# Kernel optimization log

Hardware: AMD Instinct MI355X
Metric: run time of the kernel (lower is better)

The kernel has to match this reference:

```python
import jax, jax.numpy as jnp
import numpy as np

B, OBS, H, D, E, T, A = 8192, 128, 512, 512, 16, 50, 32
LOG_STD_MIN, LOG_STD_MAX = -20.0, 2.0
ACT_LIMIT = 1.0


def setup_inputs() -> dict:
    key = jax.random.key(0)
    ks = jax.random.split(key, 24)
    s = 0.05  # weight init scale for MLP weights
    f32 = jnp.float32
    return {
        "obs": jax.random.normal(ks[0], (B, OBS), f32),
        "task": jax.random.randint(ks[1], (B,), 0, T),
        "eps": jax.random.normal(ks[2], (B, A), f32),
        # backbone: obs_dim -> 512 -> 512, relu after every layer
        "bW1": jax.random.normal(ks[3], (OBS, H), f32) * s, "bb1": jnp.zeros((H,), f32),
        "bW2": jax.random.normal(ks[4], (H, H), f32) * s, "bb2": jnp.zeros((H,), f32),
        # stacked expert MLPs: 512 -> 512(relu) -> 512(identity), batched over E
        "eW1": jax.random.normal(ks[5], (E, H, D), f32) * s, "eb1": jnp.zeros((E, D), f32),
        "eW2": jax.random.normal(ks[6], (E, D, D), f32) * s, "eb2": jnp.zeros((E, D), f32),
        # attention params (torch.randn init in original)
        "key_mats": jax.random.normal(ks[7], (E, D, D), f32),
        "value_mats": jax.random.normal(ks[8], (E, D, D), f32),
        "task_queries": jax.random.normal(ks[9], (T, D), f32),
        # mu tower: D -> 512(relu) -> act_dim
        "mW1": jax.random.normal(ks[10], (D, H), f32) * s, "mb1": jnp.zeros((H,), f32),
        "mW2": jax.random.normal(ks[11], (H, A), f32) * s, "mb2": jnp.zeros((A,), f32),
        # log_std tower: D -> 512(relu) -> act_dim
        "lW1": jax.random.normal(ks[12], (D, H), f32) * s, "lb1": jnp.zeros((H,), f32),
        "lW2": jax.random.normal(ks[13], (H, A), f32) * s, "lb2": jnp.zeros((A,), f32),
    }


def reference(obs, task, eps, bW1, bb1, bW2, bb2, eW1, eb1, eW2, eb2,
              key_mats, value_mats, task_queries,
              mW1, mb1, mW2, mb2, lW1, lb1, lW2, lb2):
    relu = jax.nn.relu
    # backbone (relu after both layers, incl. output_activation=activation)
    h = relu(obs @ bW1 + bb1)          # [B, H]
    h = relu(h @ bW2 + bb2)            # [B, H]
    # all experts as one batched GEMM (replaces jit.fork per-expert dispatch)
    eo = relu(jnp.einsum('bi,eij->bej', h, eW1) + eb1)   # [B, E, D]
    eo = jnp.einsum('bej,ejk->bek', eo, eW2) + eb2       # [B, E, D]
    # attention-weighted mixture of experts
    vals = jnp.einsum('bei,eij->bej', eo, value_mats)    # [B, E, D]
    keys = jnp.einsum('bei,eij->bej', eo, key_mats)      # [B, E, D]
    q = task_queries[task]                               # [B, D]
    w = jax.nn.softmax(jnp.einsum('bei,bi->be', keys, q), axis=-1)  # [B, E]
    tower = jnp.einsum('be,bei->bi', w, vals)            # [B, D]
    # squashed Gaussian head
    mu = relu(tower @ mW1 + mb1) @ mW2 + mb2             # [B, A]
    log_std = jnp.clip(relu(tower @ lW1 + lb1) @ lW2 + lb2, LOG_STD_MIN, LOG_STD_MAX)
    a = mu + jnp.exp(log_std) * eps                      # rsample with explicit noise
    # Normal log_prob of a = mu + std*eps, summed over action dim
    logp = jnp.sum(-0.5 * eps * eps - log_std - 0.5 * jnp.log(2.0 * jnp.pi), axis=-1)
    # tanh-squash correction
    logp = logp - jnp.sum(2.0 * (jnp.log(2.0) - a - jax.nn.softplus(-2.0 * a)), axis=-1)
    pi = ACT_LIMIT * jnp.tanh(a)
    return (pi, logp)
```

## Files before the change

kernel.cpp:

```cpp
#include <hip/hip_runtime.h>
#include <hip/hip_bf16.h>
#include <cstdint>


typedef _Float16 f16;
typedef _Float16 f16x4 __attribute__((ext_vector_type(4)));
typedef _Float16 f16x8 __attribute__((ext_vector_type(8)));
typedef float f32x4 __attribute__((ext_vector_type(4)));

__device__ __forceinline__ void fsplit(float x, f16& h, f16& l) {
    h = (f16)x;
    l = (f16)(x - (float)h);
}

__device__ __forceinline__ void gload16(const void* g, void* s) {
    __builtin_amdgcn_global_load_lds(
        (const __attribute__((address_space(1))) void*)g,
        (__attribute__((address_space(3))) void*)s, 16, 0, 0);
}

__global__ void split_pairs(const float* __restrict__ x, f16* __restrict__ h,
                            f16* __restrict__ l, int n4) {
    int i = blockIdx.x * 256 + threadIdx.x;
    if (i >= n4) return;
    float4 v = ((const float4*)x)[i];
    float a[4] = {v.x, v.y, v.z, v.w};
    f16x4 hh, ll;
#pragma unroll
    for (int j = 0; j < 4; ++j) { f16 hj, lj; fsplit(a[j], hj, lj); hh[j] = hj; ll[j] = lj; }
    *(f16x4*)&h[(long)i * 4] = hh;
    *(f16x4*)&l[(long)i * 4] = ll;
}

__global__ void transpose_split(const float* __restrict__ W, f16* __restrict__ Th,
                                f16* __restrict__ Tl, int K, int N, long ist, long ost) {
    __shared__ float t[32][33];
    const float* Wb = W + (long)blockIdx.z * ist;
    const int k0 = blockIdx.x * 32, n0 = blockIdx.y * 32;
    const int tid = threadIdx.x;
    const int r = tid >> 3, c4 = (tid & 7) * 4;
    float4 v = *(const float4*)&Wb[(long)(k0 + r) * N + n0 + c4];
    t[r][c4] = v.x; t[r][c4 + 1] = v.y; t[r][c4 + 2] = v.z; t[r][c4 + 3] = v.w;
    __syncthreads();
    f16x4 hh, ll;
#pragma unroll
    for (int j = 0; j < 4; ++j) { f16 hj, lj; fsplit(t[c4 + j][r], hj, lj); hh[j] = hj; ll[j] = lj; }
    long ob = (long)blockIdx.z * ost + (long)(n0 + r) * K + k0 + c4;
    *(f16x4*)&Th[ob] = hh;
    *(f16x4*)&Tl[ob] = ll;
}

__global__ void build_w2t(const float* __restrict__ mW2, const float* __restrict__ lW2,
                          float* __restrict__ W2T) {
    const int i = blockIdx.x * 256 + threadIdx.x;
    const int half = i >> 14, col = (i >> 9) & 31, k = i & 511;
    const float* src = half ? lW2 : mW2;
    W2T[i] = src[k * 32 + col];
}

__global__ void build_bcat(const float* __restrict__ mb1, const float* __restrict__ lb1,
                           float* __restrict__ bcat) {
    const int i = blockIdx.x * 256 + threadIdx.x;
    bcat[i] = (i < 512) ? mb1[i] : lb1[i - 512];
}

template <int OUTM, bool RELU, int AMODE, bool BSINGLE>
__global__ __launch_bounds__(256, AMODE == 0 ? 3 : 4) void gemm_pair(
    const f16* __restrict__ Ah, const f16* __restrict__ Al, int lda, long zsA,
    const f16* __restrict__ Bh, const f16* __restrict__ Bl, int ldb, long zsB,
    const float* __restrict__ bias, long zsBias,
    f16* __restrict__ Ch, f16* __restrict__ Cl, float* __restrict__ Cf,
    int ldc, long zsC, int K,
    const float* __restrict__ wscale,
    const int* __restrict__ task, const float* __restrict__ KQ2,
    float* __restrict__ scores) {
    __shared__ f16 As[AMODE == 0 ? 2 : 1][64][64];
    __shared__ f16 Bs[BSINGLE ? 1 : 2][128][64];
    const int z = blockIdx.z;
    Ah += (long)z * zsA;
    if constexpr (AMODE == 0) Al += (long)z * zsA;
    Bh += (long)z * zsB;
    if constexpr (!BSINGLE) Bl += (long)z * zsB;
    if (bias) bias += (long)z * zsBias;
    if (OUTM <= 1) { Ch += (long)z * zsC; Cl += (long)z * zsC; }
    if (OUTM == 7) { Ch += (long)z * zsC; }
    if (OUTM == 2 || OUTM == 3 || OUTM == 6) { Cf += (long)z * zsC; }
    const int tid = threadIdx.x;
    const int l = tid & 63;
    const int w = tid >> 6;
    const int row0 = blockIdx.x * 64;
    const int col0 = blockIdx.y * 128;
    const int wr = (w >> 1) * 32;
    const int wc = (w & 1) * 64;
    const int grow = l >> 3;
    const int gch = (l & 7) ^ grow;

    f32x4 acc[2][4];
#pragma unroll
    for (int mi = 0; mi < 2; ++mi)
#pragma unroll
        for (int ni = 0; ni < 4; ++ni)
#pragma unroll
            for (int j = 0; j < 4; ++j) acc[mi][ni][j] = 0.f;

    uint4 areg0, areg1; float ascl0, ascl1;
    auto ldA = [&](int k0) {
        const int r0 = w * 16 + grow, r1 = r0 + 8;
        const int scl = l & 7;
        areg0 = *(const uint4*)&Ah[(long)(row0 + r0) * lda + k0 + scl * 8];
        areg1 = *(const uint4*)&Ah[(long)(row0 + r1) * lda + k0 + scl * 8];
        const int e = k0 >> 9;
        ascl0 = wscale[(long)(row0 + r0) * 16 + e];
        ascl1 = wscale[(long)(row0 + r1) * 16 + e];
    };
    auto wrA = [&]() {
        const int scl = l & 7;
#pragma unroll
        for (int h = 0; h < 2; ++h) {
            const int r = w * 16 + grow + h * 8;
            const float s = h ? ascl1 : ascl0;
            f16x8 v = h ? *(f16x8*)&areg1 : *(f16x8*)&areg0;
#pragma unroll
            for (int j = 0; j < 8; ++j) v[j] = (f16)((float)v[j] * s);
            *(uint4*)&As[0][r][(scl ^ (r & 7)) * 8] = *(uint4*)&v;
        }
    };

    if constexpr (AMODE == 2) ldA(0);
    for (int k0 = 0; k0 < K; k0 += 64) {
        __syncthreads();
        if constexpr (AMODE == 2) {
            wrA();
            if (k0 + 64 < K) ldA(k0 + 64);
        } else {
            const long ga = (long)(row0 + w * 16 + grow) * lda + k0 + gch * 8;
            gload16(Ah + ga, &As[0][w * 16][0]);
            gload16(Ah + ga + (long)8 * lda, &As[0][w * 16 + 8][0]);
            if constexpr (AMODE == 0) {
                gload16(Al + ga, &As[1][w * 16][0]);
                gload16(Al + ga + (long)8 * lda, &As[1][w * 16 + 8][0]);
            }
        }
        {
            const long gb = (long)(col0 + w * 32 + grow) * ldb + k0 + gch * 8;
            gload16(Bh + gb, &Bs[0][w * 32][0]);
            gload16(Bh + gb + (long)8 * ldb, &Bs[0][w * 32 + 8][0]);
            gload16(Bh + gb + (long)16 * ldb, &Bs[0][w * 32 + 16][0]);
            gload16(Bh + gb + (long)24 * ldb, &Bs[0][w * 32 + 24][0]);
            if constexpr (!BSINGLE) {
                gload16(Bl + gb, &Bs[1][w * 32][0]);
                gload16(Bl + gb + (long)8 * ldb, &Bs[1][w * 32 + 8][0]);
                gload16(Bl + gb + (long)16 * ldb, &Bs[1][w * 32 + 16][0]);
                gload16(Bl + gb + (long)24 * ldb, &Bs[1][w * 32 + 24][0]);
            }
        }
        __syncthreads();
        const int r16 = l & 15, kg = l >> 4;
#pragma unroll
        for (int ks = 0; ks < 2; ++ks) {
            f16x8 a_h[2], a_l[2], b_h[4], b_l[4];
#pragma unroll
            for (int mi = 0; mi < 2; ++mi) {
                const int r = wr + mi * 16 + r16;
                const int off = ((ks * 4 + kg) ^ (r & 7)) * 8;
                a_h[mi] = *(const f16x8*)&As[0][r][off];
                if constexpr (AMODE == 0) a_l[mi] = *(const f16x8*)&As[1][r][off];
            }
#pragma unroll
            for (int ni = 0; ni < 4; ++ni) {
                const int c = wc + ni * 16 + r16;
                const int off = ((ks * 4 + kg) ^ (c & 7)) * 8;
                b_h[ni] = *(const f16x8*)&Bs[0][c][off];
                if constexpr (!BSINGLE) b_l[ni] = *(const f16x8*)&Bs[1][c][off];
            }
#pragma unroll
            for (int mi = 0; mi < 2; ++mi)
#pragma unroll
                for (int ni = 0; ni < 4; ++ni) {
                    acc[mi][ni] = __builtin_amdgcn_mfma_f32_16x16x32_f16(a_h[mi], b_h[ni], acc[mi][ni], 0, 0, 0);
                    if constexpr (!BSINGLE)
                        acc[mi][ni] = __builtin_amdgcn_mfma_f32_16x16x32_f16(a_h[mi], b_l[ni], acc[mi][ni], 0, 0, 0);
                    if constexpr (AMODE == 0)
                        acc[mi][ni] = __builtin_amdgcn_mfma_f32_16x16x32_f16(a_l[mi], b_h[ni], acc[mi][ni], 0, 0, 0);
                }
        }
    }
    const int lane15 = l & 15;
    const int rsub = (l >> 4) * 4;
    if (OUTM == 5) {
        const int expert = col0 >> 9;
        float bv[4];
#pragma unroll
        for (int ni = 0; ni < 4; ++ni)
            bv[ni] = bias ? bias[col0 + wc + ni * 16 + lane15] : 0.f;
#pragma unroll
        for (int mi = 0; mi < 2; ++mi)
#pragma unroll
            for (int j = 0; j < 4; ++j) {
                const int rowg = row0 + wr + mi * 16 + rsub + j;
                const int t = task[rowg];
                const float* kqr = KQ2 + ((long)t * 16 + expert) * 512;
                float part = 0.f;
#pragma unroll
                for (int ni = 0; ni < 4; ++ni) {
                    const int colg = col0 + wc + ni * 16 + lane15;
                    float v = acc[mi][ni][j] + bv[ni];
                    if (RELU) v = fmaxf(v, 0.f);
                    Ch[(long)rowg * ldc + colg] = (f16)v;
                    part += v * kqr[colg & 511];
                }
#pragma unroll
                for (int d = 1; d < 16; d <<= 1) part += __shfl_xor(part, d);
                if (lane15 == 0) atomicAdd(&scores[rowg * 16 + expert], part);
            }
    } else {
#pragma unroll
        for (int mi = 0; mi < 2; ++mi)
#pragma unroll
            for (int ni = 0; ni < 4; ++ni) {
                const int colg = col0 + wc + ni * 16 + lane15;
                const float bv = bias ? bias[colg] : 0.f;
#pragma unroll
                for (int j = 0; j < 4; ++j) {
                    const int rowg = row0 + wr + mi * 16 + rsub + j;
                    float v = acc[mi][ni][j] + bv;
                    if (RELU) v = fmaxf(v, 0.f);
                    if (OUTM == 0) {
                        f16 hh, ll; fsplit(v, hh, ll);
                        const long idx = (long)rowg * ldc + colg;
                        Ch[idx] = hh; Cl[idx] = ll;
                    } else if (OUTM == 1) {
                        f16 hh, ll; fsplit(v, hh, ll);
                        const long idx = (long)colg * ldc + rowg;
                        Ch[idx] = hh; Cl[idx] = ll;
                    } else if (OUTM == 2) {
                        Cf[(long)rowg * ldc + colg] = v;
                    } else if (OUTM == 3) {
                        Cf[(long)rowg * ldc + colg] += v;
                    } else if (OUTM == 6) {
                        Cf[(long)colg * ldc + rowg] = v;
                    } else if (OUTM == 7) {
                        Ch[(long)colg * ldc + rowg] = (f16)v;
                    } else if (OUTM == 8) {
                        const long idx = (long)rowg * ldc + colg;
                        v += Cf[idx];
                        Ch[idx] = (f16)v;
                    }
                }
            }
    }
}

__global__ void cb_from_kq(const f16* __restrict__ KqT_h, const f16* __restrict__ KqT_l,
                           const float* __restrict__ eb2, float* __restrict__ cb) {
    const int gw = (blockIdx.x * 256 + threadIdx.x) >> 6;
    const int l = threadIdx.x & 63;
    const int t = gw >> 4, e = gw & 15;
    const long base = (long)t * 8192 + e * 512 + l * 8;
    f16x8 hh = *(const f16x8*)&KqT_h[base];
    f16x8 ll = *(const f16x8*)&KqT_l[base];
    const float* bb = eb2 + e * 512 + l * 8;
    float s = 0.f;
#pragma unroll
    for (int j = 0; j < 8; ++j) s += ((float)hh[j] + (float)ll[j]) * bb[j];
#pragma unroll
    for (int d = 1; d < 64; d <<= 1) s += __shfl_xor(s, d);
    if (l == 0) cb[t * 16 + e] = s;
}

__global__ void bias_fold(const float* __restrict__ bvec, const float* __restrict__ M,
                          float* __restrict__ out) {
    const int gid = blockIdx.x * 256 + threadIdx.x;
    const int e = gid >> 9, j = gid & 511;
    const float* Me = M + (long)e * 262144;
    const float* be = bvec + e * 512;
    float s = 0.f;
    for (int k = 0; k < 512; ++k) s += be[k] * Me[(long)k * 512 + j];
    out[gid] = s;
}

__global__ void scores_init(const int* __restrict__ task, const float* __restrict__ cb,
                            float* __restrict__ sc) {
    const int i = blockIdx.x * 256 + threadIdx.x;
    sc[i] = cb[task[i >> 4] * 16 + (i & 15)];
}

__global__ void softmax16(float* __restrict__ sc) {
    const int b = blockIdx.x * 256 + threadIdx.x;
    float v[16];
    const float4* pp = (const float4*)&sc[b * 16];
#pragma unroll
    for (int qq = 0; qq < 4; ++qq) {
        float4 t = pp[qq];
        v[qq * 4] = t.x; v[qq * 4 + 1] = t.y; v[qq * 4 + 2] = t.z; v[qq * 4 + 3] = t.w;
    }
    float m = v[0];
#pragma unroll
    for (int e = 1; e < 16; ++e) m = fmaxf(m, v[e]);
    float ssum = 0.f;
#pragma unroll
    for (int e = 0; e < 16; ++e) { v[e] = expf(v[e] - m); ssum += v[e]; }
    const float inv = 1.f / ssum;
    float4* o = (float4*)&sc[b * 16];
#pragma unroll
    for (int qq = 0; qq < 4; ++qq) {
        float4 t;
        t.x = v[qq * 4] * inv; t.y = v[qq * 4 + 1] * inv;
        t.z = v[qq * 4 + 2] * inv; t.w = v[qq * 4 + 3] * inv;
        o[qq] = t;
    }
}

__global__ void wb_init(const float* __restrict__ w, const float* __restrict__ b2V,
                        float* __restrict__ towerAcc) {
    const int b = blockIdx.x;
    const int tid = threadIdx.x;
    float wv[16];
#pragma unroll
    for (int e = 0; e < 16; ++e) wv[e] = w[b * 16 + e];
#pragma unroll
    for (int rep = 0; rep < 2; ++rep) {
        const int j = rep * 256 + tid;
        float s = 0.f;
#pragma unroll
        for (int e = 0; e < 16; ++e) s += wv[e] * b2V[e * 512 + j];
        towerAcc[(long)b * 512 + j] = s;
    }
}

__global__ void head_kernel2(
    const f16* __restrict__ Rh, const f16* __restrict__ Rl,
    const float* __restrict__ W2T,
    const float* __restrict__ mb2, const float* __restrict__ lb2,
    const float* __restrict__ eps, float* __restrict__ pi, float* __restrict__ logp) {
    __shared__ float src[4][1032];
    const int tid = threadIdx.x, l = tid & 63, w = tid >> 6;
    const int b = blockIdx.x * 4 + w;
    const long rb = (long)b * 1024;
    {
        f16x8 h0 = *(const f16x8*)&Rh[rb + l * 8];
        f16x8 l0 = *(const f16x8*)&Rl[rb + l * 8];
        f16x8 h1 = *(const f16x8*)&Rh[rb + 512 + l * 8];
        f16x8 l1 = *(const f16x8*)&Rl[rb + 512 + l * 8];
#pragma unroll
        for (int j = 0; j < 8; ++j) {
            src[w][l * 8 + j] = (float)h0[j] + (float)l0[j];
            src[w][512 + l * 8 + j] = (float)h1[j] + (float)l1[j];
        }
    }
    __syncthreads();
    const int col = l & 31;
    const int half = l >> 5;
    const float4* wp = (const float4*)(W2T + ((long)(half * 32 + col)) * 512);
    const float4* sp = (const float4*)(&src[w][half * 512]);
    float a0 = 0.f, a1 = 0.f, a2 = 0.f, a3 = 0.f;
#pragma unroll 8
    for (int k4 = 0; k4 < 128; ++k4) {
        const float4 wv = wp[k4];
        const float4 sv = sp[k4];
        a0 = fmaf(wv.x, sv.x, a0);
        a1 = fmaf(wv.y, sv.y, a1);
        a2 = fmaf(wv.z, sv.z, a2);
        a3 = fmaf(wv.w, sv.w, a3);
    }
    const float* b2 = half ? lb2 : mb2;
    float s = b2[col] + ((a0 + a1) + (a2 + a3));
    const float other = __shfl_xor(s, 32);
    if (half == 0) {
        const float mu = s;
        float ls = fminf(fmaxf(other, -20.f), 2.f);
        const float e = eps[(long)b * 32 + col];
        const float a = mu + expf(ls) * e;
        float lt = -0.5f * e * e - ls - 0.91893853320467274f;
        const float x = -2.f * a;
        const float sp2 = fmaxf(x, 0.f) + log1pf(expf(-fabsf(x)));
        lt -= 2.f * (0.69314718055994531f - a - sp2);
        pi[(long)b * 32 + col] = tanhf(a);
        float r = lt;
#pragma unroll
        for (int d = 1; d < 32; d <<= 1) r += __shfl_xor(r, d);
        if (col == 0) logp[b] = r;
    }
}

extern "C" void kernel_launch(void* const* d_in, const int* in_sizes, int n_in,
                              void* d_out, int out_size, void* d_ws, size_t ws_size,
                              hipStream_t stream) {
    const float* obs = (const float*)d_in[0];
    const int* task = (const int*)d_in[1];
    const float* eps = (const float*)d_in[2];
    const float* bW1 = (const float*)d_in[3];
    const float* bb1 = (const float*)d_in[4];
    const float* bW2 = (const float*)d_in[5];
    const float* bb2 = (const float*)d_in[6];
    const float* eW1 = (const float*)d_in[7];
    const float* eb1 = (const float*)d_in[8];
    const float* eW2 = (const float*)d_in[9];
    const float* eb2 = (const float*)d_in[10];
    const float* keyM = (const float*)d_in[11];
    const float* valM = (const float*)d_in[12];
    const float* tq = (const float*)d_in[13];
    const float* mW1 = (const float*)d_in[14];
    const float* mb1 = (const float*)d_in[15];
    const float* mW2 = (const float*)d_in[16];
    const float* mb2 = (const float*)d_in[17];
    const float* lW1 = (const float*)d_in[18];
    const float* lb1 = (const float*)d_in[19];
    const float* lW2 = (const float*)d_in[20];
    const float* lb2 = (const float*)d_in[21];
    (void)in_sizes; (void)n_in; (void)out_size; (void)ws_size;

    const size_t MB = 1u << 20, KB = 1u << 10;
    char* base = (char*)d_ws;
    f16* eW1t_h = (f16*)(base + 0 * MB);   f16* eW1t_l = (f16*)(base + 8 * MB);
    f16* Wv2_h  = (f16*)(base + 16 * MB);
    f16* eW2s_h = (f16*)(base + 32 * MB);  f16* eW2s_l = (f16*)(base + 40 * MB);
    f16* h2_h   = (f16*)(base + 32 * MB);  f16* h2_l   = (f16*)(base + 40 * MB);
    f16* t1_h   = (f16*)(base + 48 * MB);  f16* t1_l   = (f16*)(base + 56 * MB);
    f16* Rcat_l = (f16*)(base + 48 * MB);
    f16* Vt_h   = (f16*)(base + 64 * MB);  f16* Vt_l   = (f16*)(base + 72 * MB);
    f16* Rcat_h = (f16*)(base + 64 * MB);
    f16* keyMs_h = (f16*)(base + 80 * MB); f16* keyMs_l = (f16*)(base + 88 * MB);
    f16* KqT_h   = (f16*)(base + 96 * MB); f16* KqT_l   = (f16*)(base + 98 * MB);
    f16* tqP_h   = (f16*)(base + 100 * MB); f16* tqP_l  = (f16*)(base + 100 * MB + 128 * KB);
    float* KQ2   = (float*)(base + 104 * MB);
    float* towerAcc = (float*)(base + 80 * MB);
    f16* twP_h  = (f16*)(base + 96 * MB);
    f16* obs_h  = (f16*)(base + 112 * MB); f16* obs_l  = (f16*)(base + 114 * MB);
    char* q = base + 116 * MB;
    f16* bW1t_h = (f16*)q; q += 128 * KB;  f16* bW1t_l = (f16*)q; q += 128 * KB;
    f16* bW2t_h = (f16*)q; q += 512 * KB;  f16* bW2t_l = (f16*)q; q += 512 * KB;
    f16* mW1t_h = (f16*)q; q += 512 * KB;
    f16* lW1t_h = (f16*)q; q += 512 * KB;
    f16* mW1t_l = (f16*)q; q += 512 * KB;
    f16* lW1t_l = (f16*)q; q += 512 * KB;
    float* scores = (float*)q; q += 512 * KB;
    float* b2V    = (float*)q; q += 32 * KB;
    float* cb     = (float*)q; q += 16 * KB;
    float* W2T    = (float*)q; q += 128 * KB;
    float* bcat   = (float*)q; q += 16 * KB;
    f16* U = (f16*)(base + 122 * MB);

    const long EST = 262144;

    split_pairs<<<1024, 256, 0, stream>>>(obs, obs_h, obs_l, 262144);
    split_pairs<<<4096, 256, 0, stream>>>(eW2, eW2s_h, eW2s_l, 1048576);
    split_pairs<<<4096, 256, 0, stream>>>(keyM, keyMs_h, keyMs_l, 1048576);
    hipMemsetAsync(tqP_h, 0, 256 * KB, stream);
    split_pairs<<<25, 256, 0, stream>>>(tq, tqP_h, tqP_l, 6400);
    transpose_split<<<dim3(4, 16, 1), 256, 0, stream>>>(bW1, bW1t_h, bW1t_l, 128, 512, 0, 0);
    transpose_split<<<dim3(16, 16, 1), 256, 0, stream>>>(bW2, bW2t_h, bW2t_l, 512, 512, 0, 0);
    transpose_split<<<dim3(16, 16, 1), 256, 0, stream>>>(mW1, mW1t_h, mW1t_l, 512, 512, 0, 0);
    transpose_split<<<dim3(16, 16, 1), 256, 0, stream>>>(lW1, lW1t_h, lW1t_l, 512, 512, 0, 0);
    transpose_split<<<dim3(16, 16, 16), 256, 0, stream>>>(eW1, eW1t_h, eW1t_l, 512, 512, EST, EST);
    transpose_split<<<dim3(16, 16, 16), 256, 0, stream>>>(valM, Vt_h, Vt_l, 512, 512, EST, EST);
    build_w2t<<<128, 256, 0, stream>>>(mW2, lW2, W2T);
    build_bcat<<<4, 256, 0, stream>>>(mb1, lb1, bcat);

    gemm_pair<7, false, 0, true><<<dim3(8, 4, 16), 256, 0, stream>>>(
        eW2s_h, eW2s_l, 512, EST, Vt_h, nullptr, 512, EST, nullptr, 0,
        Wv2_h, nullptr, nullptr, 8192, 512, 512, nullptr, nullptr, nullptr, nullptr);
    gemm_pair<1, false, 0, false><<<dim3(128, 1, 1), 256, 0, stream>>>(
        keyMs_h, keyMs_l, 512, 0, tqP_h, tqP_l, 512, 0, nullptr, 0,
        KqT_h, KqT_l, nullptr, 8192, 0, 512, nullptr, nullptr, nullptr, nullptr);
    gemm_pair<6, false, 0, false><<<dim3(8, 1, 16), 256, 0, stream>>>(
        eW2s_h, eW2s_l, 512, EST, KqT_h, KqT_l, 8192, 512, nullptr, 0,
        nullptr, nullptr, KQ2, 8192, 512, 512, nullptr, nullptr, nullptr, nullptr);
    cb_from_kq<<<200, 256, 0, stream>>>(KqT_h, KqT_l, eb2, cb);
    bias_fold<<<32, 256, 0, stream>>>(eb2, valM, b2V);

    gemm_pair<0, true, 0, false><<<dim3(128, 4, 1), 256, 0, stream>>>(
        obs_h, obs_l, 128, 0, bW1t_h, bW1t_l, 128, 0, bb1, 0,
        t1_h, t1_l, nullptr, 512, 0, 128, nullptr, nullptr, nullptr, nullptr);
    gemm_pair<0, true, 0, false><<<dim3(128, 4, 1), 256, 0, stream>>>(
        t1_h, t1_l, 512, 0, bW2t_h, bW2t_l, 512, 0, bb2, 0,
        h2_h, h2_l, nullptr, 512, 0, 512, nullptr, nullptr, nullptr, nullptr);

    scores_init<<<512, 256, 0, stream>>>(task, cb, scores);
    gemm_pair<5, true, 0, false><<<dim3(128, 64, 1), 256, 0, stream>>>(
        h2_h, h2_l, 512, 0, eW1t_h, eW1t_l, 512, 0, eb1, 0,
        U, nullptr, nullptr, 8192, 0, 512, nullptr, task, KQ2, scores);
    softmax16<<<32, 256, 0, stream>>>(scores);

    wb_init<<<8192, 256, 0, stream>>>(scores, b2V, towerAcc);
    gemm_pair<8, false, 2, true><<<dim3(128, 4, 1), 256, 0, stream>>>(
        U, nullptr, 8192, 0, Wv2_h, nullptr, 8192, 0, nullptr, 0,
        twP_h, nullptr, towerAcc, 512, 0, 8192, scores, nullptr, nullptr, nullptr);

    gemm_pair<0, true, 1, true><<<dim3(128, 4, 2), 256, 0, stream>>>(
        twP_h, nullptr, 512, 0, mW1t_h, nullptr, 512, 262144, bcat, 512,
        Rcat_h, Rcat_l, nullptr, 1024, 512, 512, nullptr, nullptr, nullptr, nullptr);
    head_kernel2<<<2048, 256, 0, stream>>>(Rcat_h, Rcat_l, W2T, mb2, lb2, eps,
                                           (float*)d_out, (float*)d_out + 262144);
}
```

Before: 663.9 us.

## Double-buffer GEMM LDS tiles with K=32 steps and packed two-row swizzled layout

```diff
diff --git a/kernel.cpp b/kernel.cpp
--- a/kernel.cpp
+++ b/kernel.cpp
@@ -65,7 +65,7 @@
 }
 
 template <int OUTM, bool RELU, int AMODE, bool BSINGLE>
-__global__ __launch_bounds__(256, AMODE == 0 ? 3 : 4) void gemm_pair(
+__global__ __launch_bounds__(256, (AMODE == 0 && !BSINGLE) ? 3 : 4) void gemm_pair(
     const f16* __restrict__ Ah, const f16* __restrict__ Al, int lda, long zsA,
     const f16* __restrict__ Bh, const f16* __restrict__ Bl, int ldb, long zsB,
     const float* __restrict__ bias, long zsBias,
@@ -74,8 +74,10 @@
     const float* __restrict__ wscale,
     const int* __restrict__ task, const float* __restrict__ KQ2,
     float* __restrict__ scores) {
-    __shared__ f16 As[AMODE == 0 ? 2 : 1][64][64];
-    __shared__ f16 Bs[BSINGLE ? 1 : 2][128][64];
+    constexpr int APL = (AMODE == 0) ? 2 : 1;
+    constexpr int BPL = BSINGLE ? 1 : 2;
+    __shared__ f16 As[2][APL][2048];
+    __shared__ f16 Bs[2][BPL][4096];
     const int z = blockIdx.z;
     Ah += (long)z * zsA;
     if constexpr (AMODE == 0) Al += (long)z * zsA;
@@ -92,8 +94,6 @@
     const int col0 = blockIdx.y * 128;
     const int wr = (w >> 1) * 32;
     const int wc = (w & 1) * 64;
-    const int grow = l >> 3;
-    const int gch = (l & 7) ^ grow;
 
     f32x4 acc[2][4];
 #pragma unroll
@@ -103,88 +103,125 @@
 #pragma unroll
             for (int j = 0; j < 4; ++j) acc[mi][ni][j] = 0.f;
 
-    uint4 areg0, areg1; float ascl0, ascl1;
+    auto stageA = [&](int buf, int k0) {
+        if constexpr (AMODE == 0) {
+            const int p = w >> 1;
+            const f16* src = p ? Al : Ah;
+#pragma unroll
+            for (int i = 0; i < 2; ++i) {
+                const int sr0 = (w & 1) * 16 + i * 8;
+                const int sr = sr0 + (l >> 3);
+                const int j = (l & 7) ^ (sr & 7);
+                const int row = 2 * sr + (j >> 2);
+                gload16(src + (long)(row0 + row) * lda + k0 + (j & 3) * 8,
+                        &As[buf][p][sr0 * 64]);
+            }
+        } else if constexpr (AMODE == 1) {
+            const int sr0 = w * 8;
+            const int sr = sr0 + (l >> 3);
+            const int j = (l & 7) ^ (sr & 7);
+            const int row = 2 * sr + (j >> 2);
+            gload16(Ah + (long)(row0 + row) * lda + k0 + (j & 3) * 8,
+                    &As[buf][0][sr0 * 64]);
+        }
+    };
+    auto stageB = [&](int buf, int k0) {
+        if constexpr (!BSINGLE) {
+            const int p = w >> 1;
+            const f16* src = p ? Bl : Bh;
+#pragma unroll
+            for (int i = 0; i < 4; ++i) {
+                const int sr0 = (w & 1) * 32 + i * 8;
+                const int sr = sr0 + (l >> 3);
+                const int j = (l & 7) ^ (sr & 7);
+                const int row = 2 * sr + (j >> 2);
+                gload16(src + (long)(col0 + row) * ldb + k0 + (j & 3) * 8,
+                        &Bs[buf][p][sr0 * 64]);
+            }
+        } else {
+#pragma unroll
+            for (int i = 0; i < 2; ++i) {
+                const int sr0 = w * 16 + i * 8;
+                const int sr = sr0 + (l >> 3);
+                const int j = (l & 7) ^ (sr & 7);
+                const int row = 2 * sr + (j >> 2);
+                gload16(Bh + (long)(col0 + row) * ldb + k0 + (j & 3) * 8,
+                        &Bs[buf][0][sr0 * 64]);
+            }
+        }
+    };
+    uint4 areg; float ascl;
     auto ldA = [&](int k0) {
-        const int r0 = w * 16 + grow, r1 = r0 + 8;
-        const int scl = l & 7;
-        areg0 = *(const uint4*)&Ah[(long)(row0 + r0) * lda + k0 + scl * 8];
-        areg1 = *(const uint4*)&Ah[(long)(row0 + r1) * lda + k0 + scl * 8];
-        const int e = k0 >> 9;
-        ascl0 = wscale[(long)(row0 + r0) * 16 + e];
-        ascl1 = wscale[(long)(row0 + r1) * 16 + e];
+        const int sr = tid >> 3;
+        const int j = (tid & 7) ^ (sr & 7);
+        const int row = 2 * sr + (j >> 2);
+        areg = *(const uint4*)&Ah[(long)(row0 + row) * lda + k0 + (j & 3) * 8];
+        ascl = wscale[(long)(row0 + row) * 16 + (k0 >> 9)];
     };
-    auto wrA = [&]() {
-        const int scl = l & 7;
-#pragma unroll
-        for (int h = 0; h < 2; ++h) {
-            const int r = w * 16 + grow + h * 8;
-            const float s = h ? ascl1 : ascl0;
-            f16x8 v = h ? *(f16x8*)&areg1 : *(f16x8*)&areg0;
-#pragma unroll
-            for (int j = 0; j < 8; ++j) v[j] = (f16)((float)v[j] * s);
-            *(uint4*)&As[0][r][(scl ^ (r & 7)) * 8] = *(uint4*)&v;
-        }
+    auto wrA = [&](int buf) {
+        const int sr = tid >> 3;
+        f16x8 v = *(f16x8*)&areg;
+#pragma unroll
+        for (int jj = 0; jj < 8; ++jj) v[jj] = (f16)((float)v[jj] * ascl);
+        *(uint4*)&As[buf][0][sr * 64 + (tid & 7) * 8] = *(uint4*)&v;
     };
 
-    if constexpr (AMODE == 2) ldA(0);
-    for (int k0 = 0; k0 < K; k0 += 64) {
+    auto compute = [&](int buf) {
+        const int r16 = l & 15, kg = l >> 4;
+        f16x8 a_h[2], a_l[2], b_h[4], b_l[4];
+#pragma unroll
+        for (int mi = 0; mi < 2; ++mi) {
+            const int r = wr + mi * 16 + r16;
+            const int sr = r >> 1;
+            const int off = sr * 64 + ((((r & 1) * 4 + kg) ^ (sr & 7)) << 3);
+            a_h[mi] = *(const f16x8*)&As[buf][0][off];
+            if constexpr (AMODE == 0) a_l[mi] = *(const f16x8*)&As[buf][APL - 1][off];
+        }
+#pragma unroll
+        for (int ni = 0; ni < 4; ++ni) {
+            const int c = wc + ni * 16 + r16;
+            const int sr = c >> 1;
+            const int off = sr * 64 + ((((c & 1) * 4 + kg) ^ (sr & 7)) << 3);
+            b_h[ni] = *(const f16x8*)&Bs[buf][0][off];
+            if constexpr (!BSINGLE) b_l[ni] = *(const f16x8*)&Bs[buf][BPL - 1][off];
+        }
+#pragma unroll
+        for (int mi = 0; mi < 2; ++mi)
+#pragma unroll
+            for (int ni = 0; ni < 4; ++ni) {
+                acc[mi][ni] = __builtin_amdgcn_mfma_f32_16x16x32_f16(a_h[mi], b_h[ni], acc[mi][ni], 0, 0, 0);
+                if constexpr (!BSINGLE)
+                    acc[mi][ni] = __builtin_amdgcn_mfma_f32_16x16x32_f16(a_h[mi], b_l[ni], acc[mi][ni], 0, 0, 0);
+                if constexpr (AMODE == 0)
+                    acc[mi][ni] = __builtin_amdgcn_mfma_f32_16x16x32_f16(a_l[mi], b_h[ni], acc[mi][ni], 0, 0, 0);
+            }
+    };
+
+    if constexpr (AMODE == 2) {
+        ldA(0); stageB(0, 0); wrA(0);
+        if (32 < K) ldA(32);
         __syncthreads();
-        if constexpr (AMODE == 2) {
-            wrA();
-            if (k0 + 64 < K) ldA(k0 + 64);
-        } else {
-            const long ga = (long)(row0 + w * 16 + grow) * lda + k0 + gch * 8;
-            gload16(Ah + ga, &As[0][w * 16][0]);
-            gload16(Ah + ga + (long)8 * lda, &As[0][w * 16 + 8][0]);
-            if constexpr (AMODE == 0) {
-                gload16(Al + ga, &As[1][w * 16][0]);
-                gload16(Al + ga + (long)8 * lda, &As[1][w * 16 + 8][0]);
-            }
-        }
-        {
-            const long gb = (long)(col0 + w * 32 + grow) * ldb + k0 + gch * 8;
-            gload16(Bh + gb, &Bs[0][w * 32][0]);
-            gload16(Bh + gb + (long)8 * ldb, &Bs[0][w * 32 + 8][0]);
-            gload16(Bh + gb + (long)16 * ldb, &Bs[0][w * 32 + 16][0]);
-            gload16(Bh + gb + (long)24 * ldb, &Bs[0][w * 32 + 24][0]);
-            if constexpr (!BSINGLE) {
-                gload16(Bl + gb, &Bs[1][w * 32][0]);
-                gload16(Bl + gb + (long)8 * ldb, &Bs[1][w * 32 + 8][0]);
-                gload16(Bl + gb + (long)16 * ldb, &Bs[1][w * 32 + 16][0]);
-                gload16(Bl + gb + (long)24 * ldb, &Bs[1][w * 32 + 24][0]);
-            }
-        }
+        for (int t = 0, k0 = 0; k0 < K; ++t, k0 += 32) {
+            const int nk = k0 + 32;
+            if (nk < K) {
+                stageB((t & 1) ^ 1, nk);
+                wrA((t & 1) ^ 1);
+                if (nk + 32 < K) ldA(nk + 32);
+            }
+            compute(t & 1);
+            __syncthreads();
+        }
+    } else {
+        stageA(0, 0); stageB(0, 0);
         __syncthreads();
-        const int r16 = l & 15, kg = l >> 4;
-#pragma unroll
-        for (int ks = 0; ks < 2; ++ks) {
-            f16x8 a_h[2], a_l[2], b_h[4], b_l[4];
-#pragma unroll
-            for (int mi = 0; mi < 2; ++mi) {
-                const int r = wr + mi * 16 + r16;
-                const int off = ((ks * 4 + kg) ^ (r & 7)) * 8;
-                a_h[mi] = *(const f16x8*)&As[0][r][off];
-                if constexpr (AMODE == 0) a_l[mi] = *(const f16x8*)&As[1][r][off];
-            }
-#pragma unroll
-            for (int ni = 0; ni < 4; ++ni) {
-                const int c = wc + ni * 16 + r16;
-                const int off = ((ks * 4 + kg) ^ (c & 7)) * 8;
-                b_h[ni] = *(const f16x8*)&Bs[0][c][off];
-                if constexpr (!BSINGLE) b_l[ni] = *(const f16x8*)&Bs[1][c][off];
-            }
-#pragma unroll
-            for (int mi = 0; mi < 2; ++mi)
-#pragma unroll
-                for (int ni = 0; ni < 4; ++ni) {
-                    acc[mi][ni] = __builtin_amdgcn_mfma_f32_16x16x32_f16(a_h[mi], b_h[ni], acc[mi][ni], 0, 0, 0);
-                    if constexpr (!BSINGLE)
-                        acc[mi][ni] = __builtin_amdgcn_mfma_f32_16x16x32_f16(a_h[mi], b_l[ni], acc[mi][ni], 0, 0, 0);
-                    if constexpr (AMODE == 0)
-                        acc[mi][ni] = __builtin_amdgcn_mfma_f32_16x16x32_f16(a_l[mi], b_h[ni], acc[mi][ni], 0, 0, 0);
-                }
-        }
-    }
+        for (int t = 0, k0 = 0; k0 < K; ++t, k0 += 32) {
+            const int nk = k0 + 32;
+            if (nk < K) { stageA((t & 1) ^ 1, nk); stageB((t & 1) ^ 1, nk); }
+            compute(t & 1);
+            __syncthreads();
+        }
+    }
+
     const int lane15 = l & 15;
     const int rsub = (l >> 4) * 4;
     if (OUTM == 5) {
```

Result: slower. 777.1 us (+17.0%).
